# Kernel tuning notes

Hardware: AMD Instinct MI355X
Metric: run time of the kernel (lower is better)

Reference implementation:

```python
import jax, jax.numpy as jnp
import numpy as np
import math

E = 4096  # embed_dim
H = 32    # num_heads
M = 256   # max_queries
B = 8     # batch
N = 256   # kv tokens (16x16 grid -> no pos-embed interpolation branch)


def _sincos_1d(d, pos):
    omega = np.arange(d // 2, dtype=np.float32) / (d / 2.0)
    omega = 1.0 / 10000 ** omega
    out = np.einsum('m,d->md', pos.reshape(-1), omega)
    return np.concatenate([np.sin(out), np.cos(out)], axis=1)


def _sincos_2d(embed_dim, grid_size):
    gh = np.arange(grid_size, dtype=np.float32)
    gw = np.arange(grid_size, dtype=np.float32)
    grid = np.stack(np.meshgrid(gw, gh), axis=0).reshape(2, -1)
    return np.concatenate([
        _sincos_1d(embed_dim // 2, grid[0]),
        _sincos_1d(embed_dim // 2, grid[1]),
    ], axis=1)


def setup_inputs() -> dict:
    key = jax.random.key(0)
    ks = jax.random.split(key, 4)
    grid_size = int(math.ceil(math.sqrt(M)))
    pe = _sincos_2d(E, grid_size)[:M].astype(np.float32)
    return {
        'x': jax.random.normal(ks[0], (B, N, E), jnp.float32),
        'query': 0.02 * jax.random.normal(ks[1], (M, E), jnp.float32),
        'pos_embed': jnp.asarray(pe),
        'ln_q_w': jnp.ones((E,), jnp.float32),
        'ln_q_b': jnp.zeros((E,), jnp.float32),
        'ln_kv_w': jnp.ones((E,), jnp.float32),
        'ln_kv_b': jnp.zeros((E,), jnp.float32),
        'in_proj_w': 0.02 * jax.random.normal(ks[2], (3 * E, E), jnp.float32),
        'in_proj_b': jnp.zeros((3 * E,), jnp.float32),
        'out_proj_w': 0.02 * jax.random.normal(ks[3], (E, E), jnp.float32),
        'out_proj_b': jnp.zeros((E,), jnp.float32),
    }


def _ln(x, w, b, eps=1e-5):
    m = jnp.mean(x, -1, keepdims=True)
    v = jnp.mean((x - m) ** 2, -1, keepdims=True)
    return (x - m) * jax.lax.rsqrt(v + eps) * w + b


def reference(x, query, pos_embed, ln_q_w, ln_q_b, ln_kv_w, ln_kv_b,
              in_proj_w, in_proj_b, out_proj_w, out_proj_b):
    D = E // H
    kv = _ln(x, ln_kv_w, ln_kv_b)                      # [B,N,E] (kv_proj is Identity)
    q_in = _ln(query, ln_q_w, ln_q_b) + pos_embed      # [M,E] (Q + posQ, shared over batch)
    k_in = kv + pos_embed[None]                        # N == M so posK == pos_embed (no interp)
    Wq, Wk, Wv = in_proj_w[:E], in_proj_w[E:2 * E], in_proj_w[2 * E:]
    bq, bk, bv = in_proj_b[:E], in_proj_b[E:2 * E], in_proj_b[2 * E:]
    q = (q_in @ Wq.T + bq).reshape(M, H, D).transpose(1, 0, 2)          # [H,M,D]
    k = (k_in @ Wk.T + bk).reshape(B, N, H, D).transpose(0, 2, 1, 3)    # [B,H,N,D]
    v = (kv @ Wv.T + bv).reshape(B, N, H, D).transpose(0, 2, 1, 3)      # [B,H,N,D]
    scores = jnp.einsum('hmd,bhnd->bhmn', q, k) / jnp.sqrt(jnp.float32(D))
    attn = jax.nn.softmax(scores, axis=-1)                              # [B,H,M,N]
    o = jnp.einsum('bhmn,bhnd->bhmd', attn, v)
    o = o.transpose(0, 2, 1, 3).reshape(B, M, E)
    out = o @ out_proj_w.T + out_proj_b                                 # [B,M,E]
    # need_weights=True with average_attn_weights=True -> head-averaged weights
    return out, attn.mean(axis=1)
```

## Files before the change

kernel.cpp:

```cpp
#include <hip/hip_runtime.h>
#include <hip/hip_bf16.h>

typedef __bf16 bf16;
typedef __attribute__((ext_vector_type(8))) __bf16 bf16x8;
typedef __attribute__((ext_vector_type(4))) __bf16 bf16x4;
typedef __attribute__((ext_vector_type(4))) float floatx4;

#define E_DIM 4096
#define H_DIM 32
#define D_DIM 128
#define M_DIM 256
#define B_DIM 8
#define N_DIM 256

#define GLD_LDS(g, l) __builtin_amdgcn_global_load_lds( \
    (const __attribute__((address_space(1))) unsigned int*)(g), \
    (__attribute__((address_space(3))) unsigned int*)(l), 16, 0, 0)

__device__ __forceinline__ float wave_sum(float v) {
#pragma unroll
  for (int o = 32; o; o >>= 1) v += __shfl_xor(v, o);
  return v;
}
__device__ __forceinline__ float wave_max(float v) {
#pragma unroll
  for (int o = 32; o; o >>= 1) v = fmaxf(v, __shfl_xor(v, o));
  return v;
}

#define BAR256() asm volatile("s_barrier" ::: "memory")
#define LGKM0_256()                                      \
  asm volatile("s_waitcnt lgkmcnt(0)" ::: "memory");     \
  __builtin_amdgcn_sched_barrier(0)

#define STAGE_A256(T, h)                                                       \
  {                                                                            \
    _Pragma("unroll") for (int j = 0; j < 2; ++j)                              \
        GLD_LDS(Ag + (size_t)((h)*128 + sgrow + j * 8) * lda + (T) * 64 + sgcol, \
                AsP + ((T)&1) * 16384 + (h)*8192 + sdst + j * 512);            \
  }
#define STAGE_B256(T, h)                                                       \
  {                                                                            \
    _Pragma("unroll") for (int j = 0; j < 2; ++j)                              \
        GLD_LDS(Bg + (size_t)((h)*128 + sgrow + j * 8) * ldb + (T) * 64 + sgcol, \
                BsP + ((T)&1) * 16384 + (h)*8192 + sdst + j * 512);            \
  }
#define LDA256(mh)                                                             \
  {                                                                            \
    _Pragma("unroll") for (int m = 0; m < 4; ++m) {                            \
      a[m][0] = *(const bf16x8*)(AsP + buf + rA + ((mh)*4 + m) * 1024 + slot0); \
      a[m][1] = *(const bf16x8*)(AsP + buf + rA + ((mh)*4 + m) * 1024 + slot1); \
    }                                                                          \
  }
#define LDB256(dst, nh)                                                        \
  {                                                                            \
    _Pragma("unroll") for (int n = 0; n < 2; ++n) {                            \
      dst[n][0] = *(const bf16x8*)(BsP + buf + rB + ((nh)*2 + n) * 1024 + slot0); \
      dst[n][1] = *(const bf16x8*)(BsP + buf + rB + ((nh)*2 + n) * 1024 + slot1); \
    }                                                                          \
  }
#define MFMAQ(mb, nb, B)                                                       \
  {                                                                            \
    _Pragma("unroll") for (int m = 0; m < 4; ++m)                              \
        _Pragma("unroll") for (int n = 0; n < 2; ++n) {                        \
      acc[(mb) + m][(nb) + n] = __builtin_amdgcn_mfma_f32_16x16x32_bf16(       \
          a[m][0], B[n][0], acc[(mb) + m][(nb) + n], 0, 0, 0);                 \
      acc[(mb) + m][(nb) + n] = __builtin_amdgcn_mfma_f32_16x16x32_bf16(       \
          a[m][1], B[n][1], acc[(mb) + m][(nb) + n], 0, 0, 0);                 \
    }                                                                          \
  }

__device__ __forceinline__ void gemm256_core(const bf16* __restrict__ Ag,
                                             const bf16* __restrict__ Bg,
                                             int lda, int ldb, int nkt,
                                             bf16* AsP, bf16* BsP,
                                             floatx4 (&acc)[8][4],
                                             int wid, int lane) {
  const int wm = wid >> 2, wn = wid & 3;
  const int l15 = lane & 15, q = lane >> 4, e7 = lane & 7;
  const int slot0 = ((q ^ e7) & 7) * 8;
  const int slot1 = (((4 + q) ^ e7) & 7) * 8;
  const int rA = (wm * 128 + l15) * 64;
  const int rB = (wn * 64 + l15) * 64;
  const int sgrow = wid * 16 + (lane >> 3);
  const int sgcol = ((lane & 7) ^ (lane >> 3)) * 8;
  const int sdst = wid * 1024;

  bf16x8 a[4][2], b0[2][2], b1[2][2];

  STAGE_B256(0, 0); STAGE_B256(0, 1);
  STAGE_A256(0, 0); STAGE_A256(0, 1);
  STAGE_B256(1, 0); STAGE_B256(1, 1);

  for (int U = 0; U < nkt; ++U) {
    const int buf = (U & 1) * 16384;
    if (U + 1 < nkt)
      asm volatile("s_waitcnt vmcnt(4)\n\ts_barrier" ::: "memory");
    else
      asm volatile("s_waitcnt vmcnt(0)\n\ts_barrier" ::: "memory");
    LDA256(0); LDB256(b0, 0);
    if (U + 1 < nkt) { STAGE_A256(U + 1, 0); }
    BAR256(); LGKM0_256();
    __builtin_amdgcn_s_setprio(1); MFMAQ(0, 0, b0); __builtin_amdgcn_s_setprio(0);
    __builtin_amdgcn_sched_barrier(0); BAR256();
    LDB256(b1, 1);
    if (U + 1 < nkt) { STAGE_A256(U + 1, 1); }
    BAR256(); LGKM0_256();
    __builtin_amdgcn_s_setprio(1); MFMAQ(0, 2, b1); __builtin_amdgcn_s_setprio(0);
    __builtin_amdgcn_sched_barrier(0); BAR256();
    LDA256(1);
    if (U + 2 < nkt) { STAGE_B256(U + 2, 0); }
    BAR256(); LGKM0_256();
    __builtin_amdgcn_s_setprio(1); MFMAQ(4, 2, b1); __builtin_amdgcn_s_setprio(0);
    __builtin_amdgcn_sched_barrier(0); BAR256();
    if (U + 2 < nkt) { STAGE_B256(U + 2, 1); }
    BAR256();
    __builtin_amdgcn_s_setprio(1); MFMAQ(4, 0, b0); __builtin_amdgcn_s_setprio(0);
    __builtin_amdgcn_sched_barrier(0);
  }
}

__global__ __launch_bounds__(512, 1)
void proj256(const bf16* __restrict__ qin, const bf16* __restrict__ kin,
             const bf16* __restrict__ kv, const bf16* __restrict__ Wqkv,
             const float* __restrict__ bqkv, float* __restrict__ qpart,
             bf16* __restrict__ kp, bf16* __restrict__ vt) {
  __shared__ __align__(16) bf16 As2[32768];
  __shared__ __align__(16) bf16 Bs2[32768];
  const int tid = threadIdx.x, wid = tid >> 6, lane = tid & 63;

  const int o = blockIdx.x;
  const int id = (o & 7) * 32 + (o >> 3);
  int role, bx, by;
  const bf16 *A, *B;
  const float* bias;
  bf16* C;
  if (id < 128) {
    role = 1; by = id & 7; bx = id >> 3;
    A = kin; B = Wqkv + 16777216; bias = bqkv + 4096; C = kp;
  } else {
    role = 2; by = (id - 128) & 7; bx = (id - 128) >> 3;
    A = kv; B = Wqkv + 33554432; bias = bqkv + 8192; C = vt;
  }
  const int trowA = by * 256, trowB = bx * 256;
  const bf16* Ag = A + (size_t)trowA * E_DIM;
  const bf16* Bg = B + (size_t)trowB * E_DIM;

  floatx4 acc[8][4];
#pragma unroll
  for (int i = 0; i < 8; ++i)
#pragma unroll
    for (int j = 0; j < 4; ++j) acc[i][j] = (floatx4){0.f, 0.f, 0.f, 0.f};

  gemm256_core(Ag, Bg, E_DIM, E_DIM, 64, As2, Bs2, acc, wid, lane);

  const int wm = wid >> 2, wn = wid & 3;
  const int l15 = lane & 15, q = lane >> 4;
  const int mrow0 = trowA + wm * 128 + q * 4;
  const int ncol0 = trowB + wn * 64 + l15;
  if (role == 1) {
#pragma unroll
    for (int m = 0; m < 8; ++m)
#pragma unroll
      for (int n = 0; n < 4; ++n) {
        const int col = ncol0 + n * 16;
        const float bb = bias[col];
        floatx4 v = acc[m][n];
#pragma unroll
        for (int r = 0; r < 4; ++r)
          C[(size_t)(mrow0 + m * 16 + r) * E_DIM + col] = (bf16)(v[r] + bb);
      }
  } else {
#pragma unroll
    for (int m = 0; m < 8; ++m)
#pragma unroll
      for (int n = 0; n < 4; ++n) {
        const int col = ncol0 + n * 16;
        const int h = col >> 7, d = col & 127;
        const float bb = bias[col];
        const int row0 = mrow0 + m * 16;
        const int b_ = row0 >> 8, n_ = row0 & 255;
        floatx4 v = acc[m][n];
        bf16x4 p;
#pragma unroll
        for (int r = 0; r < 4; ++r) p[r] = (bf16)(v[r] + bb);
        *(bf16x4*)(C + ((size_t)((b_ * H_DIM + h) * D_DIM + d)) * N_DIM + n_) = p;
      }
  }

  const int qx = id & 15, kc = id >> 4;
  const bf16* Agq = qin + kc * 256;
  const bf16* Bgq = Wqkv + (size_t)(qx * 256) * E_DIM + kc * 256;
#pragma unroll
  for (int i = 0; i < 8; ++i)
#pragma unroll
    for (int j = 0; j < 4; ++j) acc[i][j] = (floatx4){0.f, 0.f, 0.f, 0.f};

  gemm256_core(Agq, Bgq, E_DIM, E_DIM, 4, As2, Bs2, acc, wid, lane);

  float* qdst = qpart + (size_t)kc * 1048576;
  const int qmrow0 = wm * 128 + q * 4;
  const int qncol0 = qx * 256 + wn * 64 + l15;
#pragma unroll
  for (int m = 0; m < 8; ++m)
#pragma unroll
    for (int n = 0; n < 4; ++n) {
      const int col = qncol0 + n * 16;
      floatx4 v = acc[m][n];
#pragma unroll
      for (int r = 0; r < 4; ++r)
        qdst[(size_t)(qmrow0 + m * 16 + r) * E_DIM + col] = v[r];
    }
}

__global__ __launch_bounds__(256) void qreduce_kernel(const float* __restrict__ qpart,
                                                      const float* __restrict__ bias,
                                                      bf16* __restrict__ qp) {
  const size_t i = ((size_t)blockIdx.x * 256 + threadIdx.x) * 4;
  float4 s = *(const float4*)(bias + (i & 4095));
#pragma unroll
  for (int kc = 0; kc < 16; ++kc) {
    float4 v = *(const float4*)(qpart + (size_t)kc * 1048576 + i);
    s.x += v.x; s.y += v.y; s.z += v.z; s.w += v.w;
  }
  bf16x4 p; p[0] = (bf16)s.x; p[1] = (bf16)s.y; p[2] = (bf16)s.z; p[3] = (bf16)s.w;
  *(bf16x4*)(qp + i) = p;
}

__global__ __launch_bounds__(512, 1)
void scores256(const bf16* __restrict__ qp, const bf16* __restrict__ kp,
               float* __restrict__ scores, float scale) {
  __shared__ __align__(16) bf16 As2[32768];
  __shared__ __align__(16) bf16 Bs2[32768];
  const int tid = threadIdx.x, wid = tid >> 6, lane = tid & 63;

  const int o = blockIdx.x;
  const int z = (o & 7) * 32 + (o >> 3);
  const int zb = z >> 5, zh = z & 31;
  const bf16* Ag = qp + zh * D_DIM;
  const bf16* Bg = kp + (size_t)zb * N_DIM * E_DIM + zh * D_DIM;

  floatx4 acc[8][4];
#pragma unroll
  for (int i = 0; i < 8; ++i)
#pragma unroll
    for (int j = 0; j < 4; ++j) acc[i][j] = (floatx4){0.f, 0.f, 0.f, 0.f};

  gemm256_core(Ag, Bg, E_DIM, E_DIM, 2, As2, Bs2, acc, wid, lane);

  const int wm = wid >> 2, wn = wid & 3;
  const int l15 = lane & 15, q = lane >> 4;
  const int mrow0 = wm * 128 + q * 4;
  const int ncol0 = wn * 64 + l15;
  float* Cz = scores + (size_t)z * (M_DIM * N_DIM);
#pragma unroll
  for (int m = 0; m < 8; ++m)
#pragma unroll
    for (int n = 0; n < 4; ++n) {
      const int col = ncol0 + n * 16;
      floatx4 v = acc[m][n];
#pragma unroll
      for (int r = 0; r < 4; ++r)
        Cz[(size_t)(mrow0 + m * 16 + r) * N_DIM + col] = v[r] * scale;
    }
}

__global__ __launch_bounds__(512, 1)
void outproj256(const bf16* __restrict__ obuf, const bf16* __restrict__ Wout,
                float* __restrict__ Cf) {
  __shared__ __align__(16) bf16 As2[32768];
  __shared__ __align__(16) bf16 Bs2[32768];
  const int tid = threadIdx.x, wid = tid >> 6, lane = tid & 63;

  const int o = blockIdx.x;
  const int id = (o & 7) * 32 + (o >> 3);
  const int z = id >> 7;
  const int t = id & 127;
  const int by = t & 7, bx = t >> 3;
  const int trowA = by * 256, trowB = bx * 256;
  const bf16* Ag = obuf + (size_t)z * 2048 + (size_t)trowA * E_DIM;
  const bf16* Bg = Wout + (size_t)z * 2048 + (size_t)trowB * E_DIM;

  floatx4 acc[8][4];
#pragma unroll
  for (int i = 0; i < 8; ++i)
#pragma unroll
    for (int j = 0; j < 4; ++j) acc[i][j] = (floatx4){0.f, 0.f, 0.f, 0.f};

  gemm256_core(Ag, Bg, E_DIM, E_DIM, 32, As2, Bs2, acc, wid, lane);

  const int wm = wid >> 2, wn = wid & 3;
  const int l15 = lane & 15, q = lane >> 4;
  const int mrow0 = trowA + wm * 128 + q * 4;
  const int ncol0 = trowB + wn * 64 + l15;
#pragma unroll
  for (int m = 0; m < 8; ++m)
#pragma unroll
    for (int n = 0; n < 4; ++n) {
      const int col = ncol0 + n * 16;
      floatx4 v = acc[m][n];
#pragma unroll
      for (int r = 0; r < 4; ++r)
        Cf[(size_t)z * 8388608 + (size_t)(mrow0 + m * 16 + r) * E_DIM + col] = v[r];
    }
}

__device__ __forceinline__ void gemm_core_small(const bf16* __restrict__ Arow,
                                                const bf16* __restrict__ Brow,
                                                int lda, int ldb, int kTiles,
                                                bf16* As, bf16* Bs,
                                                floatx4 (&acc)[4][4],
                                                int wid, int lane) {
  const int s0 = wid * 2;
  const int lp = lane ^ ((lane >> 3) & 7);
  const int srow = lp >> 2;
  const int skoff = (lp & 3) * 8;
  const int rA = (wid >> 1) * 64 + (lane & 15);
  const int rB = (wid & 1) * 64 + (lane & 15);
  const int q16 = (lane >> 4) * 8;
  const int ex = (((lane & 15) >> 1) & 7) << 3;

#pragma unroll
  for (int c = 0; c < 2; ++c) {
    const int s = s0 + c;
    const int row = s * 16 + srow;
    GLD_LDS(Arow + (size_t)row * lda + skoff, As + s * 512);
    GLD_LDS(Brow + (size_t)row * ldb + skoff, Bs + s * 512);
  }

  for (int kt = 0; kt < kTiles; ++kt) {
    const int cur = (kt & 1) * 4096;
    const int nxt = 4096 - cur;
    __syncthreads();
    if (kt + 1 < kTiles) {
      const int k0 = (kt + 1) << 5;
#pragma unroll
      for (int c = 0; c < 2; ++c) {
        const int s = s0 + c;
        const int row = s * 16 + srow;
        GLD_LDS(Arow + (size_t)row * lda + k0 + skoff, As + nxt + s * 512);
        GLD_LDS(Brow + (size_t)row * ldb + k0 + skoff, Bs + nxt + s * 512);
      }
    }
    bf16x8 af[4], bfr[4];
#pragma unroll
    for (int t = 0; t < 4; ++t) {
      af[t] = *(const bf16x8*)(As + cur + ((((rA + t * 16) * 32) + q16) ^ ex));
      bfr[t] = *(const bf16x8*)(Bs + cur + ((((rB + t * 16) * 32) + q16) ^ ex));
    }
#pragma unroll
    for (int tr = 0; tr < 4; ++tr)
#pragma unroll
      for (int tc = 0; tc < 4; ++tc)
        acc[tr][tc] = __builtin_amdgcn_mfma_f32_16x16x32_bf16(af[tr], bfr[tc],
                                                              acc[tr][tc], 0, 0, 0);
  }
}

__global__ __launch_bounds__(256) void prep_kernel(
    const float* __restrict__ x, const float* __restrict__ lnxw,
    const float* __restrict__ lnxb, const float* __restrict__ pos,
    bf16* __restrict__ kv, bf16* __restrict__ kin,
    const float* __restrict__ qsrc, const float* __restrict__ lnqw,
    const float* __restrict__ lnqb, bf16* __restrict__ qin,
    const float* __restrict__ Wqkv_f, bf16* __restrict__ Wqkv,
    const float* __restrict__ Wout_f, bf16* __restrict__ Wout) {
  const int bid = blockIdx.x;
  const int tid = threadIdx.x, wid = tid >> 6, lane = tid & 63;

  if (bid >= 2304) {
    const int cb = bid - 2304;
#pragma unroll
    for (int c = 0; c < 8; ++c) {
      long i = (((long)c * 4096 + cb) * 256 + tid) * 8;
      const float* src;
      bf16* dst;
      if (i < 50331648L) { src = Wqkv_f + i; dst = Wqkv + i; }
      else { src = Wout_f + (i - 50331648L); dst = Wout + (i - 50331648L); }
      float4 a = *(const float4*)(src);
      float4 b = *(const float4*)(src + 4);
      bf16x8 p;
      p[0] = (bf16)a.x; p[1] = (bf16)a.y; p[2] = (bf16)a.z; p[3] = (bf16)a.w;
      p[4] = (bf16)b.x; p[5] = (bf16)b.y; p[6] = (bf16)b.z; p[7] = (bf16)b.w;
      *(bf16x8*)(dst) = p;
    }
    return;
  }

  const bool is_q = (bid >= 2048);
  const int row = is_q ? (bid - 2048) : bid;
  const float* xr = (is_q ? qsrc : x) + (size_t)row * E_DIM;
  const float* w = is_q ? lnqw : lnxw;
  const float* bvec = is_q ? lnqb : lnxb;
  const int posrow = is_q ? row : (row & (N_DIM - 1));

  float4 v[4];
  float s1 = 0.f, s2 = 0.f;
#pragma unroll
  for (int j = 0; j < 4; ++j) {
    v[j] = *(const float4*)(xr + j * 1024 + tid * 4);
    s1 += v[j].x + v[j].y + v[j].z + v[j].w;
    s2 += v[j].x * v[j].x + v[j].y * v[j].y + v[j].z * v[j].z + v[j].w * v[j].w;
  }
  s1 = wave_sum(s1); s2 = wave_sum(s2);
  __shared__ float red[8];
  if (lane == 0) { red[wid] = s1; red[wid + 4] = s2; }
  __syncthreads();
  s1 = red[0] + red[1] + red[2] + red[3];
  s2 = red[4] + red[5] + red[6] + red[7];
  const float mean = s1 * (1.f / E_DIM);
  const float var = s2 * (1.f / E_DIM) - mean * mean;
  const float rs = rsqrtf(var + 1e-5f);
#pragma unroll
  for (int j = 0; j < 4; ++j) {
    const int idx = j * 1024 + tid * 4;
    float4 wv = *(const float4*)(w + idx);
    float4 bv = *(const float4*)(bvec + idx);
    float4 pv = *(const float4*)(pos + (size_t)posrow * E_DIM + idx);
    float y0 = (v[j].x - mean) * rs * wv.x + bv.x;
    float y1 = (v[j].y - mean) * rs * wv.y + bv.y;
    float y2 = (v[j].z - mean) * rs * wv.z + bv.z;
    float y3 = (v[j].w - mean) * rs * wv.w + bv.w;
    if (is_q) {
      bf16x4 a;
      a[0] = (bf16)(y0 + pv.x); a[1] = (bf16)(y1 + pv.y);
      a[2] = (bf16)(y2 + pv.z); a[3] = (bf16)(y3 + pv.w);
      *(bf16x4*)(qin + (size_t)row * E_DIM + idx) = a;
    } else {
      bf16x4 a; a[0] = (bf16)y0; a[1] = (bf16)y1; a[2] = (bf16)y2; a[3] = (bf16)y3;
      *(bf16x4*)(kv + (size_t)row * E_DIM + idx) = a;
      bf16x4 c; c[0] = (bf16)(y0 + pv.x); c[1] = (bf16)(y1 + pv.y);
      c[2] = (bf16)(y2 + pv.z); c[3] = (bf16)(y3 + pv.w);
      *(bf16x4*)(kin + (size_t)row * E_DIM + idx) = c;
    }
  }
}

template <int MODE>
__global__ __launch_bounds__(256, 2)
void gemm_bt(const bf16* __restrict__ Abase, const bf16* __restrict__ Bbase,
             float* __restrict__ Cf, bf16* __restrict__ Cb,
             int K, int lda, int ldb, int ldc, float scale) {
  __shared__ __align__(16) bf16 As[8192];
  __shared__ __align__(16) bf16 Bs[8192];
  const int tid = threadIdx.x;
  const int wid = tid >> 6;
  const int lane = tid & 63;

  const bf16* A = Abase;
  const bf16* B = Bbase;
  if constexpr (MODE == 3) {
    int z = blockIdx.z;
    A += (size_t)z * M_DIM * 512;
    B += (size_t)z * D_DIM * N_DIM;
  }

  const bf16* Arow = A + (size_t)(blockIdx.y * 128) * lda;
  const bf16* Brow = B + (size_t)(blockIdx.x * 128) * ldb;

  floatx4 acc[4][4];
#pragma unroll
  for (int i = 0; i < 4; ++i)
#pragma unroll
    for (int j = 0; j < 4; ++j) acc[i][j] = (floatx4){0.f, 0.f, 0.f, 0.f};

  gemm_core_small(Arow, Brow, lda, ldb, K >> 5, As, Bs, acc, wid, lane);

  const int mb = blockIdx.y * 128 + (wid >> 1) * 64 + (lane >> 4) * 4;
  const int nb = blockIdx.x * 128 + (wid & 1) * 64 + (lane & 15);
#pragma unroll
  for (int tr = 0; tr < 4; ++tr) {
#pragma unroll
    for (int tc = 0; tc < 4; ++tc) {
      const int row0 = mb + tr * 16;
      const int col = nb + tc * 16;
      floatx4 a = acc[tr][tc];
      int z = blockIdx.z; int zb_ = z >> 5, zh_ = z & 31;
#pragma unroll
      for (int r = 0; r < 4; ++r)
        Cb[(size_t)zb_ * M_DIM * E_DIM + (size_t)(row0 + r) * E_DIM + zh_ * D_DIM + col] =
            (bf16)a[r];
    }
  }
}

__global__ __launch_bounds__(256) void reduce_out_kernel(const float* __restrict__ p,
                                                         const float* __restrict__ bias,
                                                         float* __restrict__ out) {
  const size_t i = ((size_t)blockIdx.x * 256 + threadIdx.x) * 4;
  float4 a = *(const float4*)(p + i);
  float4 b = *(const float4*)(p + 8388608 + i);
  float4 bb = *(const float4*)(bias + (i & 4095));
  float4 o;
  o.x = a.x + b.x + bb.x; o.y = a.y + b.y + bb.y;
  o.z = a.z + b.z + bb.z; o.w = a.w + b.w + bb.w;
  *(float4*)(out + i) = o;
}

__global__ __launch_bounds__(256) void softmax_mean_kernel(float* __restrict__ scores,
                                                           float* __restrict__ out_mean) {
  const int bm = blockIdx.x;
  const int b = bm >> 8, m = bm & 255;
  const int wid = threadIdx.x >> 6, lane = threadIdx.x & 63;
  float a0 = 0.f, a1 = 0.f, a2 = 0.f, a3 = 0.f;
  for (int j = 0; j < 8; ++j) {
    const int h = wid * 8 + j;
    float* row = scores + ((size_t)((b * H_DIM + h) * M_DIM + m)) * N_DIM;
    float4 v = *(const float4*)(row + lane * 4);
    float mx = fmaxf(fmaxf(v.x, v.y), fmaxf(v.z, v.w));
    mx = wave_max(mx);
    v.x = __expf(v.x - mx); v.y = __expf(v.y - mx);
    v.z = __expf(v.z - mx); v.w = __expf(v.w - mx);
    const float s = wave_sum(v.x + v.y + v.z + v.w);
    const float inv = 1.f / s;
    v.x *= inv; v.y *= inv; v.z *= inv; v.w *= inv;
    a0 += v.x; a1 += v.y; a2 += v.z; a3 += v.w;
    bf16x4 p; p[0] = (bf16)v.x; p[1] = (bf16)v.y; p[2] = (bf16)v.z; p[3] = (bf16)v.w;
    *(bf16x4*)((bf16*)row + lane * 4) = p;
  }
  __shared__ float red[4][256];
  *(float4*)&red[wid][lane * 4] = make_float4(a0, a1, a2, a3);
  __syncthreads();
  if (wid == 0) {
    float4 r0 = *(float4*)&red[0][lane * 4];
    float4 r1 = *(float4*)&red[1][lane * 4];
    float4 r2 = *(float4*)&red[2][lane * 4];
    float4 r3 = *(float4*)&red[3][lane * 4];
    float4 o;
    o.x = (r0.x + r1.x + r2.x + r3.x) * (1.f / H_DIM);
    o.y = (r0.y + r1.y + r2.y + r3.y) * (1.f / H_DIM);
    o.z = (r0.z + r1.z + r2.z + r3.z) * (1.f / H_DIM);
    o.w = (r0.w + r1.w + r2.w + r3.w) * (1.f / H_DIM);
    *(float4*)(out_mean + (size_t)bm * N_DIM + lane * 4) = o;
  }
}

extern "C" void kernel_launch(void* const* d_in, const int* in_sizes, int n_in,
                              void* d_out, int out_size, void* d_ws, size_t ws_size,
                              hipStream_t stream) {
  const float* x = (const float*)d_in[0];
  const float* query = (const float*)d_in[1];
  const float* pos = (const float*)d_in[2];
  const float* ln_q_w = (const float*)d_in[3];
  const float* ln_q_b = (const float*)d_in[4];
  const float* ln_kv_w = (const float*)d_in[5];
  const float* ln_kv_b = (const float*)d_in[6];
  const float* Wqkv_f = (const float*)d_in[7];
  const float* bqkv = (const float*)d_in[8];
  const float* Wout_f = (const float*)d_in[9];
  const float* bout = (const float*)d_in[10];

  char* ws = (char*)d_ws;
  bf16* Wqkv = (bf16*)(ws + 0);
  bf16* Wout = (bf16*)(ws + 100663296);
  bf16* kv   = (bf16*)(ws + 134217728);
  bf16* kin  = (bf16*)(ws + 150994944);
  bf16* qin  = (bf16*)(ws + 167772160);
  bf16* qp   = (bf16*)(ws + 169869312);
  bf16* kp   = (bf16*)(ws + 171966464);
  bf16* vt   = (bf16*)(ws + 188743680);
  float* partials = (float*)(ws + 205520896);
  float* qpart = partials;
  float* scores = (float*)(ws + 0);
  bf16* obuf = (bf16*)(ws + 67108864);

  float* out = (float*)d_out;
  float* out2 = out + (size_t)B_DIM * M_DIM * E_DIM;

  prep_kernel<<<6400, 256, 0, stream>>>(x, ln_kv_w, ln_kv_b, pos, kv, kin,
                                        query, ln_q_w, ln_q_b, qin,
                                        Wqkv_f, Wqkv, Wout_f, Wout);

  proj256<<<256, 512, 0, stream>>>(qin, kin, kv, Wqkv, bqkv, qpart, kp, vt);
  qreduce_kernel<<<1024, 256, 0, stream>>>(qpart, bqkv, qp);

  scores256<<<256, 512, 0, stream>>>(qp, kp, scores, 0.08838834764831845f);
  softmax_mean_kernel<<<2048, 256, 0, stream>>>(scores, out2);
  gemm_bt<3><<<dim3(1, 2, 256), 256, 0, stream>>>((const bf16*)scores, vt,
                                                  nullptr, obuf,
                                                  256, 512, 256, 4096, 1.f);
  outproj256<<<256, 512, 0, stream>>>(obuf, Wout, partials);
  reduce_out_kernel<<<8192, 256, 0, stream>>>(partials, bout, out);
}
```

Before: 736.9 us.

## Fuse softmax into scores GEMM epilogue and drop split-K in output projection

The scores kernel now does the softmax in its epilogue, reducing row max and sum across waves through LDS, and writes bf16 probabilities directly. This removes the fp32 score round-trip to memory and the separate softmax pass. A small kernel computes the head-averaged weights from the bf16 probabilities. The output projection switches from a 2-way split-K with a separate reduce kernel to a 128x256 tile GEMM core over the full K that adds the bias in its epilogue, removing the fp32 partial buffers. The trade-offs are more register pressure in the fused epilogue and head-mean weights computed from rounded bf16 probabilities.

```diff
diff --git a/kernel.cpp b/kernel.cpp
--- a/kernel.cpp
+++ b/kernel.cpp
@@ -20,11 +20,6 @@
 __device__ __forceinline__ float wave_sum(float v) {
 #pragma unroll
   for (int o = 32; o; o >>= 1) v += __shfl_xor(v, o);
-  return v;
-}
-__device__ __forceinline__ float wave_max(float v) {
-#pragma unroll
-  for (int o = 32; o; o >>= 1) v = fmaxf(v, __shfl_xor(v, o));
   return v;
 }
 
@@ -120,6 +115,74 @@
   }
 }
 
+#define STAGE_A128(T)                                                          \
+  {                                                                            \
+    _Pragma("unroll") for (int j = 0; j < 2; ++j)                              \
+        GLD_LDS(Ag + (size_t)(sgrow + j * 8) * lda + (T) * 64 + sgcol,         \
+                AsP + ((T)&1) * 8192 + sdst + j * 512);                        \
+  }
+#define LDA128()                                                               \
+  {                                                                            \
+    _Pragma("unroll") for (int m = 0; m < 4; ++m) {                            \
+      a[m][0] = *(const bf16x8*)(AsP + bufA + rA + m * 1024 + slot0);          \
+      a[m][1] = *(const bf16x8*)(AsP + bufA + rA + m * 1024 + slot1);          \
+    }                                                                          \
+  }
+#define MFMAH(nb, bh)                                                          \
+  {                                                                            \
+    _Pragma("unroll") for (int m = 0; m < 4; ++m) {                            \
+      acc[m][nb] = __builtin_amdgcn_mfma_f32_16x16x32_bf16(a[m][0], bh[0],     \
+                                                           acc[m][nb], 0, 0, 0); \
+      acc[m][nb] = __builtin_amdgcn_mfma_f32_16x16x32_bf16(a[m][1], bh[1],     \
+                                                           acc[m][nb], 0, 0, 0); \
+    }                                                                          \
+  }
+
+__device__ __forceinline__ void gemm128_core(const bf16* __restrict__ Ag,
+                                             const bf16* __restrict__ Bg,
+                                             int lda, int ldb, int nkt,
+                                             bf16* AsP, bf16* BsP,
+                                             floatx4 (&acc)[4][4],
+                                             int wid, int lane) {
+  const int wm = wid >> 2, wn = wid & 3;
+  const int l15 = lane & 15, q = lane >> 4, e7 = lane & 7;
+  const int slot0 = ((q ^ e7) & 7) * 8;
+  const int slot1 = (((4 + q) ^ e7) & 7) * 8;
+  const int rA = (wm * 64 + l15) * 64;
+  const int rB = (wn * 64 + l15) * 64;
+  const int sgrow = wid * 16 + (lane >> 3);
+  const int sgcol = ((lane & 7) ^ (lane >> 3)) * 8;
+  const int sdst = wid * 1024;
+
+  bf16x8 a[4][2], b0[2][2], b1[2][2];
+
+  STAGE_B256(0, 0); STAGE_B256(0, 1);
+  STAGE_A128(0);
+  STAGE_B256(1, 0); STAGE_B256(1, 1);
+
+  for (int U = 0; U < nkt; ++U) {
+    const int buf = (U & 1) * 16384;
+    const int bufA = (U & 1) * 8192;
+    if (U + 1 < nkt)
+      asm volatile("s_waitcnt vmcnt(4)\n\ts_barrier" ::: "memory");
+    else
+      asm volatile("s_waitcnt vmcnt(0)\n\ts_barrier" ::: "memory");
+    LDA128(); LDB256(b0, 0);
+    if (U + 1 < nkt) { STAGE_A128(U + 1); }
+    BAR256(); LGKM0_256();
+    __builtin_amdgcn_s_setprio(1); MFMAQ(0, 0, b0); __builtin_amdgcn_s_setprio(0);
+    __builtin_amdgcn_sched_barrier(0); BAR256();
+    LDB256(b1, 1);
+    BAR256(); LGKM0_256();
+    __builtin_amdgcn_s_setprio(1); MFMAH(2, b1[0]); __builtin_amdgcn_s_setprio(0);
+    __builtin_amdgcn_sched_barrier(0); BAR256();
+    if (U + 2 < nkt) { STAGE_B256(U + 2, 0); STAGE_B256(U + 2, 1); }
+    BAR256();
+    __builtin_amdgcn_s_setprio(1); MFMAH(3, b1[1]); __builtin_amdgcn_s_setprio(0);
+    __builtin_amdgcn_sched_barrier(0);
+  }
+}
+
 __global__ __launch_bounds__(512, 1)
 void proj256(const bf16* __restrict__ qin, const bf16* __restrict__ kin,
              const bf16* __restrict__ kv, const bf16* __restrict__ Wqkv,
@@ -228,8 +291,8 @@
 }
 
 __global__ __launch_bounds__(512, 1)
-void scores256(const bf16* __restrict__ qp, const bf16* __restrict__ kp,
-               float* __restrict__ scores, float scale) {
+void scores_sm(const bf16* __restrict__ qp, const bf16* __restrict__ kp,
+               bf16* __restrict__ probs, float scale) {
   __shared__ __align__(16) bf16 As2[32768];
   __shared__ __align__(16) bf16 Bs2[32768];
   const int tid = threadIdx.x, wid = tid >> 6, lane = tid & 63;
@@ -250,58 +313,140 @@
 
   const int wm = wid >> 2, wn = wid & 3;
   const int l15 = lane & 15, q = lane >> 4;
-  const int mrow0 = wm * 128 + q * 4;
-  const int ncol0 = wn * 64 + l15;
-  float* Cz = scores + (size_t)z * (M_DIM * N_DIM);
+
 #pragma unroll
   for (int m = 0; m < 8; ++m)
+#pragma unroll
+    for (int n = 0; n < 4; ++n) acc[m][n] *= scale;
+
+  float vmax[8][4];
+#pragma unroll
+  for (int m = 0; m < 8; ++m)
+#pragma unroll
+    for (int r = 0; r < 4; ++r)
+      vmax[m][r] = fmaxf(fmaxf(acc[m][0][r], acc[m][1][r]),
+                         fmaxf(acc[m][2][r], acc[m][3][r]));
+#pragma unroll
+  for (int mask = 1; mask < 16; mask <<= 1)
+#pragma unroll
+    for (int m = 0; m < 8; ++m)
+#pragma unroll
+      for (int r = 0; r < 4; ++r)
+        vmax[m][r] = fmaxf(vmax[m][r], __shfl_xor(vmax[m][r], mask));
+
+  float* red = (float*)As2;
+  __syncthreads();
+  if (l15 == 0) {
+#pragma unroll
+    for (int m = 0; m < 8; ++m)
+#pragma unroll
+      for (int r = 0; r < 4; ++r)
+        red[(wm * 128 + m * 16 + q * 4 + r) * 4 + wn] = vmax[m][r];
+  }
+  __syncthreads();
+  float rmax[8][4];
+#pragma unroll
+  for (int m = 0; m < 8; ++m)
+#pragma unroll
+    for (int r = 0; r < 4; ++r) {
+      const int row = wm * 128 + m * 16 + q * 4 + r;
+      rmax[m][r] = fmaxf(fmaxf(red[row * 4 + 0], red[row * 4 + 1]),
+                         fmaxf(red[row * 4 + 2], red[row * 4 + 3]));
+    }
+
+  float vsum[8][4];
+#pragma unroll
+  for (int m = 0; m < 8; ++m)
+#pragma unroll
+    for (int r = 0; r < 4; ++r) {
+      float s = 0.f;
+#pragma unroll
+      for (int n = 0; n < 4; ++n) {
+        float e = __expf(acc[m][n][r] - rmax[m][r]);
+        acc[m][n][r] = e;
+        s += e;
+      }
+      vsum[m][r] = s;
+    }
+#pragma unroll
+  for (int mask = 1; mask < 16; mask <<= 1)
+#pragma unroll
+    for (int m = 0; m < 8; ++m)
+#pragma unroll
+      for (int r = 0; r < 4; ++r)
+        vsum[m][r] += __shfl_xor(vsum[m][r], mask);
+  if (l15 == 0) {
+#pragma unroll
+    for (int m = 0; m < 8; ++m)
+#pragma unroll
+      for (int r = 0; r < 4; ++r)
+        red[1024 + (wm * 128 + m * 16 + q * 4 + r) * 4 + wn] = vsum[m][r];
+  }
+  __syncthreads();
+
+  bf16* P = probs + (size_t)z * (M_DIM * N_DIM);
+#pragma unroll
+  for (int m = 0; m < 8; ++m)
+#pragma unroll
+    for (int r = 0; r < 4; ++r) {
+      const int row = wm * 128 + m * 16 + q * 4 + r;
+      const float tot = red[1024 + row * 4 + 0] + red[1024 + row * 4 + 1] +
+                        red[1024 + row * 4 + 2] + red[1024 + row * 4 + 3];
+      const float inv = 1.f / tot;
+#pragma unroll
+      for (int n = 0; n < 4; ++n)
+        P[(size_t)row * N_DIM + wn * 64 + l15 + n * 16] =
+            (bf16)(acc[m][n][r] * inv);
+    }
+}
+
+__global__ __launch_bounds__(256) void probs_mean(const bf16* __restrict__ probs,
+                                                  float* __restrict__ out2) {
+  const int bm = blockIdx.x;
+  const int b = bm >> 8, m = bm & 255;
+  const int n = threadIdx.x;
+  float s = 0.f;
+#pragma unroll
+  for (int h = 0; h < H_DIM; ++h)
+    s += (float)probs[((size_t)(b * H_DIM + h) * M_DIM + m) * N_DIM + n];
+  out2[(size_t)bm * N_DIM + n] = s * (1.f / H_DIM);
+}
+
+__global__ __launch_bounds__(512, 1)
+void outproj128(const bf16* __restrict__ obuf, const bf16* __restrict__ Wout,
+                const float* __restrict__ bout, float* __restrict__ out) {
+  __shared__ __align__(16) bf16 As2[16384];
+  __shared__ __align__(16) bf16 Bs2[32768];
+  const int tid = threadIdx.x, wid = tid >> 6, lane = tid & 63;
+
+  const int o = blockIdx.x;
+  const int id = (o & 7) * 32 + (o >> 3);
+  const int mt = id >> 4, nt = id & 15;
+  const bf16* Ag = obuf + (size_t)(mt * 128) * E_DIM;
+  const bf16* Bg = Wout + (size_t)(nt * 256) * E_DIM;
+
+  floatx4 acc[4][4];
+#pragma unroll
+  for (int i = 0; i < 4; ++i)
+#pragma unroll
+    for (int j = 0; j < 4; ++j) acc[i][j] = (floatx4){0.f, 0.f, 0.f, 0.f};
+
+  gemm128_core(Ag, Bg, E_DIM, E_DIM, 64, As2, Bs2, acc, wid, lane);
+
+  const int wm = wid >> 2, wn = wid & 3;
+  const int l15 = lane & 15, q4 = lane >> 4;
+  const int mrow0 = mt * 128 + wm * 64 + q4 * 4;
+  const int ncol0 = nt * 256 + wn * 64 + l15;
+#pragma unroll
+  for (int m = 0; m < 4; ++m)
 #pragma unroll
     for (int n = 0; n < 4; ++n) {
       const int col = ncol0 + n * 16;
+      const float bb = bout[col];
       floatx4 v = acc[m][n];
 #pragma unroll
       for (int r = 0; r < 4; ++r)
-        Cz[(size_t)(mrow0 + m * 16 + r) * N_DIM + col] = v[r] * scale;
-    }
-}
-
-__global__ __launch_bounds__(512, 1)
-void outproj256(const bf16* __restrict__ obuf, const bf16* __restrict__ Wout,
-                float* __restrict__ Cf) {
-  __shared__ __align__(16) bf16 As2[32768];
-  __shared__ __align__(16) bf16 Bs2[32768];
-  const int tid = threadIdx.x, wid = tid >> 6, lane = tid & 63;
-
-  const int o = blockIdx.x;
-  const int id = (o & 7) * 32 + (o >> 3);
-  const int z = id >> 7;
-  const int t = id & 127;
-  const int by = t & 7, bx = t >> 3;
-  const int trowA = by * 256, trowB = bx * 256;
-  const bf16* Ag = obuf + (size_t)z * 2048 + (size_t)trowA * E_DIM;
-  const bf16* Bg = Wout + (size_t)z * 2048 + (size_t)trowB * E_DIM;
-
-  floatx4 acc[8][4];
-#pragma unroll
-  for (int i = 0; i < 8; ++i)
-#pragma unroll
-    for (int j = 0; j < 4; ++j) acc[i][j] = (floatx4){0.f, 0.f, 0.f, 0.f};
-
-  gemm256_core(Ag, Bg, E_DIM, E_DIM, 32, As2, Bs2, acc, wid, lane);
-
-  const int wm = wid >> 2, wn = wid & 3;
-  const int l15 = lane & 15, q = lane >> 4;
-  const int mrow0 = trowA + wm * 128 + q * 4;
-  const int ncol0 = trowB + wn * 64 + l15;
-#pragma unroll
-  for (int m = 0; m < 8; ++m)
-#pragma unroll
-    for (int n = 0; n < 4; ++n) {
-      const int col = ncol0 + n * 16;
-      floatx4 v = acc[m][n];
-#pragma unroll
-      for (int r = 0; r < 4; ++r)
-        Cf[(size_t)z * 8388608 + (size_t)(mrow0 + m * 16 + r) * E_DIM + col] = v[r];
+        out[(size_t)(mrow0 + m * 16 + r) * E_DIM + col] = v[r] + bb;
     }
 }
 
@@ -436,27 +581,21 @@
   }
 }
 
-template <int MODE>
 __global__ __launch_bounds__(256, 2)
-void gemm_bt(const bf16* __restrict__ Abase, const bf16* __restrict__ Bbase,
-             float* __restrict__ Cf, bf16* __restrict__ Cb,
-             int K, int lda, int ldb, int ldc, float scale) {
+void gemm_pv(const bf16* __restrict__ probs, const bf16* __restrict__ vt,
+             bf16* __restrict__ Cb) {
   __shared__ __align__(16) bf16 As[8192];
   __shared__ __align__(16) bf16 Bs[8192];
   const int tid = threadIdx.x;
   const int wid = tid >> 6;
   const int lane = tid & 63;
 
-  const bf16* A = Abase;
-  const bf16* B = Bbase;
-  if constexpr (MODE == 3) {
-    int z = blockIdx.z;
-    A += (size_t)z * M_DIM * 512;
-    B += (size_t)z * D_DIM * N_DIM;
-  }
-
-  const bf16* Arow = A + (size_t)(blockIdx.y * 128) * lda;
-  const bf16* Brow = B + (size_t)(blockIdx.x * 128) * ldb;
+  const int z = blockIdx.z;
+  const bf16* A = probs + (size_t)z * (M_DIM * N_DIM);
+  const bf16* B = vt + (size_t)z * D_DIM * N_DIM;
+
+  const bf16* Arow = A + (size_t)(blockIdx.y * 128) * N_DIM;
+  const bf16* Brow = B;
 
   floatx4 acc[4][4];
 #pragma unroll
@@ -464,10 +603,11 @@
 #pragma unroll
     for (int j = 0; j < 4; ++j) acc[i][j] = (floatx4){0.f, 0.f, 0.f, 0.f};
 
-  gemm_core_small(Arow, Brow, lda, ldb, K >> 5, As, Bs, acc, wid, lane);
+  gemm_core_small(Arow, Brow, N_DIM, N_DIM, 8, As, Bs, acc, wid, lane);
 
   const int mb = blockIdx.y * 128 + (wid >> 1) * 64 + (lane >> 4) * 4;
-  const int nb = blockIdx.x * 128 + (wid & 1) * 64 + (lane & 15);
+  const int nb = (wid & 1) * 64 + (lane & 15);
+  const int zb_ = z >> 5, zh_ = z & 31;
 #pragma unroll
   for (int tr = 0; tr < 4; ++tr) {
 #pragma unroll
@@ -475,63 +615,11 @@
       const int row0 = mb + tr * 16;
       const int col = nb + tc * 16;
       floatx4 a = acc[tr][tc];
-      int z = blockIdx.z; int zb_ = z >> 5, zh_ = z & 31;
 #pragma unroll
       for (int r = 0; r < 4; ++r)
         Cb[(size_t)zb_ * M_DIM * E_DIM + (size_t)(row0 + r) * E_DIM + zh_ * D_DIM + col] =
             (bf16)a[r];
     }
-  }
-}
-
-__global__ __launch_bounds__(256) void reduce_out_kernel(const float* __restrict__ p,
-                                                         const float* __restrict__ bias,
-                                                         float* __restrict__ out) {
-  const size_t i = ((size_t)blockIdx.x * 256 + threadIdx.x) * 4;
-  float4 a = *(const float4*)(p + i);
-  float4 b = *(const float4*)(p + 8388608 + i);
-  float4 bb = *(const float4*)(bias + (i & 4095));
-  float4 o;
-  o.x = a.x + b.x + bb.x; o.y = a.y + b.y + bb.y;
-  o.z = a.z + b.z + bb.z; o.w = a.w + b.w + bb.w;
-  *(float4*)(out + i) = o;
-}
-
-__global__ __launch_bounds__(256) void softmax_mean_kernel(float* __restrict__ scores,
-                                                           float* __restrict__ out_mean) {
-  const int bm = blockIdx.x;
-  const int b = bm >> 8, m = bm & 255;
-  const int wid = threadIdx.x >> 6, lane = threadIdx.x & 63;
-  float a0 = 0.f, a1 = 0.f, a2 = 0.f, a3 = 0.f;
-  for (int j = 0; j < 8; ++j) {
-    const int h = wid * 8 + j;
-    float* row = scores + ((size_t)((b * H_DIM + h) * M_DIM + m)) * N_DIM;
-    float4 v = *(const float4*)(row + lane * 4);
-    float mx = fmaxf(fmaxf(v.x, v.y), fmaxf(v.z, v.w));
-    mx = wave_max(mx);
-    v.x = __expf(v.x - mx); v.y = __expf(v.y - mx);
-    v.z = __expf(v.z - mx); v.w = __expf(v.w - mx);
-    const float s = wave_sum(v.x + v.y + v.z + v.w);
-    const float inv = 1.f / s;
-    v.x *= inv; v.y *= inv; v.z *= inv; v.w *= inv;
-    a0 += v.x; a1 += v.y; a2 += v.z; a3 += v.w;
-    bf16x4 p; p[0] = (bf16)v.x; p[1] = (bf16)v.y; p[2] = (bf16)v.z; p[3] = (bf16)v.w;
-    *(bf16x4*)((bf16*)row + lane * 4) = p;
-  }
-  __shared__ float red[4][256];
-  *(float4*)&red[wid][lane * 4] = make_float4(a0, a1, a2, a3);
-  __syncthreads();
-  if (wid == 0) {
-    float4 r0 = *(float4*)&red[0][lane * 4];
-    float4 r1 = *(float4*)&red[1][lane * 4];
-    float4 r2 = *(float4*)&red[2][lane * 4];
-    float4 r3 = *(float4*)&red[3][lane * 4];
-    float4 o;
-    o.x = (r0.x + r1.x + r2.x + r3.x) * (1.f / H_DIM);
-    o.y = (r0.y + r1.y + r2.y + r3.y) * (1.f / H_DIM);
-    o.z = (r0.z + r1.z + r2.z + r3.z) * (1.f / H_DIM);
-    o.w = (r0.w + r1.w + r2.w + r3.w) * (1.f / H_DIM);
-    *(float4*)(out_mean + (size_t)bm * N_DIM + lane * 4) = o;
   }
 }
 
@@ -559,9 +647,8 @@
   bf16* qp   = (bf16*)(ws + 169869312);
   bf16* kp   = (bf16*)(ws + 171966464);
   bf16* vt   = (bf16*)(ws + 188743680);
-  float* partials = (float*)(ws + 205520896);
-  float* qpart = partials;
-  float* scores = (float*)(ws + 0);
+  float* qpart = (float*)(ws + 205520896);
+  bf16* probs = (bf16*)(ws + 0);
   bf16* obuf = (bf16*)(ws + 67108864);
 
   float* out = (float*)d_out;
@@ -574,11 +661,10 @@
   proj256<<<256, 512, 0, stream>>>(qin, kin, kv, Wqkv, bqkv, qpart, kp, vt);
   qreduce_kernel<<<1024, 256, 0, stream>>>(qpart, bqkv, qp);
 
-  scores256<<<256, 512, 0, stream>>>(qp, kp, scores, 0.08838834764831845f);
-  softmax_mean_kernel<<<2048, 256, 0, stream>>>(scores, out2);
-  gemm_bt<3><<<dim3(1, 2, 256), 256, 0, stream>>>((const bf16*)scores, vt,
-                                                  nullptr, obuf,
-                                                  256, 512, 256, 4096, 1.f);
-  outproj256<<<256, 512, 0, stream>>>(obuf, Wout, partials);
-  reduce_out_kernel<<<8192, 256, 0, stream>>>(partials, bout, out);
-}
+  scores_sm<<<256, 512, 0, stream>>>(qp, kp, probs, 0.08838834764831845f);
+  probs_mean<<<2048, 256, 0, stream>>>(probs, out2);
+
+  gemm_pv<<<dim3(1, 2, 256), 256, 0, stream>>>(probs, vt, obuf);
+
+  outproj128<<<256, 512, 0, stream>>>(obuf, Wout, bout, out);
+}
```

New measurement: 722.5 us. About the same (-1.9%).
